# Kernel tuning notes

Hardware: AMD Instinct MI355X
Metric: run time of the kernel (lower is better)

Reference implementation:

```python
import jax, jax.numpy as jnp
import numpy as np

LEAKY_SLOPE = 0.01  # torch F.leaky_relu default
COS_EPS = 1e-8      # torch F.cosine_similarity default eps


def _gc(pre, cur, adj, W):
    # GraphConvolution.forward
    pre_w = pre @ W            # [N, d]
    cur_w = cur @ W            # [M, d]
    new_pre = adj @ cur_w      # [N, d]
    new_cur = adj.T @ pre_w    # [M, d]
    new_pre = jnp.where(new_pre >= 0, new_pre, LEAKY_SLOPE * new_pre)
    new_cur = jnp.where(new_cur >= 0, new_cur, LEAKY_SLOPE * new_cur)
    return new_pre, new_cur


def _cos_sim(pre, cur):
    # Fused pairwise cosine similarity: matches torch F.cosine_similarity per pair
    dots = pre @ cur.T                         # [N, M]
    n_pre = jnp.linalg.norm(pre, axis=1)       # [N]
    n_cur = jnp.linalg.norm(cur, axis=1)       # [M]
    denom = jnp.maximum(n_pre[:, None] * n_cur[None, :], COS_EPS)
    return dots / denom


def setup_inputs() -> dict:
    key = jax.random.key(0)
    k1, k2, k3, k4, k5 = jax.random.split(key, 5)
    N, d = 8192, 128
    stdv = 1.0 / np.sqrt(d)
    pre = jax.random.normal(k1, (N, d), dtype=jnp.float32)
    cur = jax.random.normal(k2, (N, d), dtype=jnp.float32)
    adj = jax.random.uniform(k3, (N, N), dtype=jnp.float32)
    W1 = jax.random.uniform(k4, (d, d), dtype=jnp.float32, minval=-stdv, maxval=stdv)
    W2 = jax.random.uniform(k5, (d, d), dtype=jnp.float32, minval=-stdv, maxval=stdv)
    return {"pre": pre, "cur": cur, "adj": adj, "W1": W1, "W2": W2}


def reference(pre, cur, adj, W1, W2):
    pre1, cur1 = _gc(pre, cur, adj, W1)
    adj1 = _cos_sim(pre1, cur1)
    pre2, cur2 = _gc(pre1, cur1, adj1, W2)
    adj2 = _cos_sim(pre2, cur2)
    return adj2
```

## Files before the change

kernel.cpp:

```cpp
#include <hip/hip_runtime.h>


#define NN 8192
#define DD 128

typedef __bf16 bf16x8 __attribute__((ext_vector_type(8)));
typedef float f32x4 __attribute__((ext_vector_type(4)));

static __device__ __forceinline__ float4 ldg4(const float* p) {
    return *reinterpret_cast<const float4*>(p);
}

static __device__ __forceinline__ unsigned f2bf2(float lo, float hi) {
    __bf16 a = (__bf16)lo, b = (__bf16)hi;
    unsigned short ua = __builtin_bit_cast(unsigned short, a);
    unsigned short ub = __builtin_bit_cast(unsigned short, b);
    return (unsigned)ua | ((unsigned)ub << 16);
}

#define FC(v, j) ((j) == 0 ? (v).x : (j) == 1 ? (v).y : (j) == 2 ? (v).z : (v).w)

#define PRAGU _Pragma("unroll")

static __device__ __forceinline__ int swz16(int row) {
    return (((row & 7) ^ ((row >> 3) & 7)) << 4);
}
static __device__ __forceinline__ int lslot(int row, int slot) {
    return ((slot & 8) << 4) | (((slot & 7) << 4) ^ swz16(row));
}

__global__ __launch_bounds__(256, 2)
void mfma_adj(const float* __restrict__ adj,
              const unsigned short* __restrict__ BTa,
              const unsigned short* __restrict__ BTb,
              float* __restrict__ C, int ksplit, int zstride)
{
    __shared__ alignas(16) char smem[65536];
    char* smA = smem;
    char* smB = smem + 32768;

    const int t    = threadIdx.x;
    const int l    = t & 63;
    const int w    = t >> 6;
    const int wr   = (w >> 1) * 64;
    const int wc   = (w & 1) * 64;
    const int lrow = l & 15;
    const int lhi  = l >> 4;
    const int i0   = blockIdx.x * 128;
    const int z    = blockIdx.z;
    const bool second = z >= 8;
    const unsigned short* BT = second ? BTb : BTa;
    const int kbase = (z & 7) * ksplit;
    C += (size_t)z * (size_t)zstride;

    const int srow = t >> 3;
    const int skg  = t & 7;
    const int u    = t & 31;
    const int r8   = t >> 5;

    f32x4 acc[4][4];
    PRAGU
    for (int r = 0; r < 4; ++r)
        PRAGU
        for (int q = 0; q < 4; ++q)
            PRAGU
            for (int e = 0; e < 4; ++e) acc[r][q][e] = 0.0f;

    const int nt = ksplit >> 7;
    for (int tc = 0; tc < nt; ++tc) {
        const int kk = kbase + tc * 128;

        PRAGU
        for (int h = 0; h < 2; ++h) {
            const int kh = kk + h * 64;
            if (second) {
                float4 rv[8];
                PRAGU
                for (int e = 0; e < 8; ++e)
                    rv[e] = ldg4(&adj[(size_t)(kh + r8 * 8 + e) * NN + i0 + u * 4]);
                PRAGU
                for (int j = 0; j < 4; ++j) {
                    const int c = u * 4 + j;
                    uint4 wv;
                    wv.x = f2bf2(FC(rv[0], j), FC(rv[1], j));
                    wv.y = f2bf2(FC(rv[2], j), FC(rv[3], j));
                    wv.z = f2bf2(FC(rv[4], j), FC(rv[5], j));
                    wv.w = f2bf2(FC(rv[6], j), FC(rv[7], j));
                    *reinterpret_cast<uint4*>(smA + c * 256 + lslot(c, h * 8 + r8)) = wv;
                }
            } else {
                PRAGU
                for (int it = 0; it < 4; ++it) {
                    const int row = it * 32 + srow;
                    const float* g = adj + (size_t)(i0 + row) * NN + kh + skg * 8;
                    float4 f0 = ldg4(g), f1 = ldg4(g + 4);
                    uint4 wv;
                    wv.x = f2bf2(f0.x, f0.y);
                    wv.y = f2bf2(f0.z, f0.w);
                    wv.z = f2bf2(f1.x, f1.y);
                    wv.w = f2bf2(f1.z, f1.w);
                    *reinterpret_cast<uint4*>(smA + row * 256 + lslot(row, h * 8 + skg)) = wv;
                }
            }
            PRAGU
            for (int it = 0; it < 4; ++it) {
                const int n = it * 32 + srow;
                *reinterpret_cast<uint4*>(smB + n * 256 + lslot(n, h * 8 + skg)) =
                    *reinterpret_cast<const uint4*>(BT + (size_t)n * NN + kh + skg * 8);
            }
        }
        __syncthreads();

        PRAGU
        for (int s = 0; s < 4; ++s) {
            bf16x8 af[4], bq[4];
            PRAGU
            for (int r = 0; r < 4; ++r) {
                const int row = wr + r * 16 + lrow;
                af[r] = *reinterpret_cast<const bf16x8*>(smA + row * 256 + lslot(row, s * 4 + lhi));
            }
            PRAGU
            for (int q = 0; q < 4; ++q) {
                const int col = wc + q * 16 + lrow;
                bq[q] = *reinterpret_cast<const bf16x8*>(smB + col * 256 + lslot(col, s * 4 + lhi));
            }
            PRAGU
            for (int r = 0; r < 4; ++r)
                PRAGU
                for (int q = 0; q < 4; ++q)
                    acc[r][q] = __builtin_amdgcn_mfma_f32_16x16x32_bf16(af[r], bq[q], acc[r][q], 0, 0, 0);
        }
        __syncthreads();
    }

    float* sC = (float*)smem;
    PRAGU
    for (int h = 0; h < 2; ++h) {
        if ((w & 1) == h) {
            PRAGU
            for (int r = 0; r < 4; ++r)
                PRAGU
                for (int q = 0; q < 4; ++q)
                    PRAGU
                    for (int i = 0; i < 4; ++i)
                        sC[(wr + r * 16 + lhi * 4 + i) * 68 + q * 16 + lrow] = acc[r][q][i];
        }
        __syncthreads();
        PRAGU
        for (int it = 0; it < 8; ++it) {
            const int idx = it * 256 + t;
            const int row = idx >> 4;
            const int c4  = (idx & 15) << 2;
            f32x4 v = *reinterpret_cast<const f32x4*>(&sC[row * 68 + c4]);
            *reinterpret_cast<f32x4*>(&C[(size_t)(i0 + row) * DD + h * 64 + c4]) = v;
        }
        __syncthreads();
    }
}

__global__ __launch_bounds__(256, 2)
void mfma_out(const unsigned short* __restrict__ A,
              const unsigned short* __restrict__ BT,
              float* __restrict__ C)
{
    __shared__ alignas(16) char smem[65536];
    char* smA = smem;
    char* smB = smem + 32768;

    const int t    = threadIdx.x;
    const int l    = t & 63;
    const int w    = t >> 6;
    const int wr   = (w >> 1) * 64;
    const int wc   = (w & 1) * 64;
    const int lrow = l & 15;
    const int lhi  = l >> 4;
    const int i0   = blockIdx.x * 128;
    const int j0   = blockIdx.y * 128;
    const int s16  = t >> 4;
    const int slot = t & 15;

    f32x4 acc[4][4];
    PRAGU
    for (int r = 0; r < 4; ++r)
        PRAGU
        for (int q = 0; q < 4; ++q)
            PRAGU
            for (int e = 0; e < 4; ++e) acc[r][q][e] = 0.0f;

    PRAGU
    for (int it = 0; it < 8; ++it) {
        const int row = it * 16 + s16;
        *reinterpret_cast<uint4*>(smA + row * 256 + lslot(row, slot)) =
            *reinterpret_cast<const uint4*>(A + (size_t)(i0 + row) * DD + slot * 8);
        *reinterpret_cast<uint4*>(smB + row * 256 + lslot(row, slot)) =
            *reinterpret_cast<const uint4*>(BT + (size_t)(j0 + row) * DD + slot * 8);
    }
    __syncthreads();

    PRAGU
    for (int s = 0; s < 4; ++s) {
        bf16x8 af[4], bq[4];
        PRAGU
        for (int r = 0; r < 4; ++r) {
            const int row = wr + r * 16 + lrow;
            af[r] = *reinterpret_cast<const bf16x8*>(smA + row * 256 + lslot(row, s * 4 + lhi));
        }
        PRAGU
        for (int q = 0; q < 4; ++q) {
            const int col = wc + q * 16 + lrow;
            bq[q] = *reinterpret_cast<const bf16x8*>(smB + col * 256 + lslot(col, s * 4 + lhi));
        }
        PRAGU
        for (int r = 0; r < 4; ++r)
            PRAGU
            for (int q = 0; q < 4; ++q)
                acc[r][q] = __builtin_amdgcn_mfma_f32_16x16x32_bf16(af[r], bq[q], acc[r][q], 0, 0, 0);
    }

    PRAGU
    for (int r = 0; r < 4; ++r)
        PRAGU
        for (int i = 0; i < 4; ++i) {
            const int grow = i0 + wr + r * 16 + lhi * 4 + i;
            float* cp = C + (size_t)grow * NN + j0 + wc;
            PRAGU
            for (int q = 0; q < 4; ++q)
                cp[q * 16 + lrow] = acc[r][q][i];
        }
}

__global__ __launch_bounds__(256, 2)
void gemm_w1t(const float* __restrict__ pre, const float* __restrict__ cur,
              const float* __restrict__ W1,
              unsigned short* __restrict__ pwT, unsigned short* __restrict__ cwT)
{
    __shared__ float sA[32][68];
    __shared__ float sB[64][128];

    const int t  = threadIdx.x;
    const int ct = t & 31;
    const int rt = t >> 5;
    const int bx = blockIdx.x;
    const bool isCur = bx >= 256;
    const float* A = isCur ? cur : pre;
    unsigned short* XT = isCur ? cwT : pwT;
    const int i0 = (bx & 255) * 32;

    float4 acc[4];
    #pragma unroll
    for (int r = 0; r < 4; ++r) { acc[r].x = 0.f; acc[r].y = 0.f; acc[r].z = 0.f; acc[r].w = 0.f; }

    for (int k0 = 0; k0 < DD; k0 += 64) {
        #pragma unroll
        for (int f = 0; f < 2; ++f) {
            const int row = (t >> 4) + 16 * f;
            const int kk4 = (t & 15) << 2;
            *reinterpret_cast<float4*>(&sA[row][kk4]) =
                ldg4(&A[(size_t)(i0 + row) * DD + k0 + kk4]);
        }
        #pragma unroll
        for (int f = 0; f < 8; ++f) {
            const int idx = f * 256 + t;
            const int kk  = idx >> 5;
            const int c4  = (idx & 31) << 2;
            *reinterpret_cast<float4*>(&sB[kk][c4]) =
                ldg4(&W1[(size_t)(k0 + kk) * DD + c4]);
        }
        __syncthreads();
        #pragma unroll 4
        for (int kk = 0; kk < 64; kk += 4) {
            float4 a[4], b[4];
            #pragma unroll
            for (int r = 0; r < 4; ++r)
                a[r] = *reinterpret_cast<const float4*>(&sA[rt * 4 + r][kk]);
            #pragma unroll
            for (int q = 0; q < 4; ++q)
                b[q] = *reinterpret_cast<const float4*>(&sB[kk + q][ct * 4]);
            #pragma unroll
            for (int r = 0; r < 4; ++r) {
                acc[r].x += a[r].x * b[0].x; acc[r].y += a[r].x * b[0].y;
                acc[r].z += a[r].x * b[0].z; acc[r].w += a[r].x * b[0].w;
                acc[r].x += a[r].y * b[1].x; acc[r].y += a[r].y * b[1].y;
                acc[r].z += a[r].y * b[1].z; acc[r].w += a[r].y * b[1].w;
                acc[r].x += a[r].z * b[2].x; acc[r].y += a[r].z * b[2].y;
                acc[r].z += a[r].z * b[2].z; acc[r].w += a[r].z * b[2].w;
                acc[r].x += a[r].w * b[3].x; acc[r].y += a[r].w * b[3].y;
                acc[r].z += a[r].w * b[3].z; acc[r].w += a[r].w * b[3].w;
            }
        }
        __syncthreads();
    }

    float* sC = &sB[0][0];
    #pragma unroll
    for (int r = 0; r < 4; ++r)
        *reinterpret_cast<float4*>(&sC[(rt * 4 + r) * 128 + ct * 4]) = acc[r];
    __syncthreads();

    const int n = t & 127;
    const int g = t >> 7;
    #pragma unroll
    for (int c = 0; c < 2; ++c) {
        const int ii = (2 * g + c) * 8;
        uint4 wv;
        wv.x = f2bf2(sC[(ii + 0) * 128 + n], sC[(ii + 1) * 128 + n]);
        wv.y = f2bf2(sC[(ii + 2) * 128 + n], sC[(ii + 3) * 128 + n]);
        wv.z = f2bf2(sC[(ii + 4) * 128 + n], sC[(ii + 5) * 128 + n]);
        wv.w = f2bf2(sC[(ii + 6) * 128 + n], sC[(ii + 7) * 128 + n]);
        *reinterpret_cast<uint4*>(&XT[(size_t)n * NN + i0 + ii]) = wv;
    }
}

__global__ __launch_bounds__(128)
void rln(const float* __restrict__ kparts, float* __restrict__ Xbase,
         float* __restrict__ invbase)
{
    const int i = blockIdx.x;
    const int y = blockIdx.y;
    const int t = threadIdx.x;
    const float* part = kparts + (size_t)(1 - y) * 8 * (NN * DD);
    float* X = Xbase + (size_t)y * (NN * DD);
    float* inv_n = invbase + y * NN;

    float s = 0.f;
    #pragma unroll
    for (int z = 0; z < 8; ++z)
        s += part[(size_t)z * (NN * DD) + (size_t)i * DD + t];
    float y_ = (s >= 0.f) ? s : 0.01f * s;
    X[(size_t)i * DD + t] = y_;
    float n = y_ * y_;
    #pragma unroll
    for (int o = 32; o > 0; o >>= 1) n += __shfl_down(n, o);
    __shared__ float p[2];
    if ((t & 63) == 0) p[t >> 6] = n;
    __syncthreads();
    if (t == 0) inv_n[i] = 1.0f / sqrtf(p[0] + p[1]);
}

template<bool TRANSA, bool SCALEK, int EPI>
__global__ __launch_bounds__(256, 2)
void gemm32(const float* __restrict__ A, int lda,
            const float* __restrict__ B, int ldb,
            float* __restrict__ C, unsigned short* __restrict__ Cb,
            int ksplit_len, int zstride,
            const float* __restrict__ kscale,
            const float* __restrict__ rscale,
            int ystA, int ystB, int ystC, int ystS)
{
    __shared__ float sA[32][68];
    __shared__ float sB[64][128];

    const int t  = threadIdx.x;
    const int ct = t & 31;
    const int rt = t >> 5;
    const int i0 = blockIdx.x * 32;
    const int side = blockIdx.y;
    const int kgbase = blockIdx.z * ksplit_len;

    A += (ptrdiff_t)side * ystA;
    B += (ptrdiff_t)side * ystB;
    if constexpr (EPI == 0)
        C += (ptrdiff_t)side * ystC + (size_t)blockIdx.z * (size_t)zstride;
    if constexpr (EPI == 3)
        Cb += (ptrdiff_t)side * ystC;
    if constexpr (SCALEK) kscale += (ptrdiff_t)side * ystS;
    if constexpr (EPI == 3) rscale += (ptrdiff_t)side * ystS;

    float4 acc[4];
    #pragma unroll
    for (int r = 0; r < 4; ++r) { acc[r].x = 0.f; acc[r].y = 0.f; acc[r].z = 0.f; acc[r].w = 0.f; }

    for (int k0 = 0; k0 < ksplit_len; k0 += 64) {
        const int kg = kgbase + k0;
        if (!TRANSA) {
            #pragma unroll
            for (int f = 0; f < 2; ++f) {
                const int row = (t >> 4) + 16 * f;
                const int kk4 = (t & 15) << 2;
                *reinterpret_cast<float4*>(&sA[row][kk4]) =
                    ldg4(&A[(size_t)(i0 + row) * lda + kg + kk4]);
            }
        } else {
            #pragma unroll
            for (int f = 0; f < 2; ++f) {
                const int kk = (t >> 3) + 32 * f;
                const int r4 = (t & 7) << 2;
                float4 v = ldg4(&A[(size_t)(kg + kk) * lda + i0 + r4]);
                if (SCALEK) {
                    const float s = kscale[kg + kk];
                    v.x *= s; v.y *= s; v.z *= s; v.w *= s;
                }
                sA[r4 + 0][kk] = v.x; sA[r4 + 1][kk] = v.y;
                sA[r4 + 2][kk] = v.z; sA[r4 + 3][kk] = v.w;
            }
        }
        #pragma unroll
        for (int f = 0; f < 8; ++f) {
            const int idx = f * 256 + t;
            const int kk  = idx >> 5;
            const int c4  = (idx & 31) << 2;
            *reinterpret_cast<float4*>(&sB[kk][c4]) =
                ldg4(&B[(size_t)(kg + kk) * ldb + c4]);
        }
        __syncthreads();
        #pragma unroll 4
        for (int kk = 0; kk < 64; kk += 4) {
            float4 a[4], b[4];
            #pragma unroll
            for (int r = 0; r < 4; ++r)
                a[r] = *reinterpret_cast<const float4*>(&sA[rt * 4 + r][kk]);
            #pragma unroll
            for (int q = 0; q < 4; ++q)
                b[q] = *reinterpret_cast<const float4*>(&sB[kk + q][ct * 4]);
            #pragma unroll
            for (int r = 0; r < 4; ++r) {
                acc[r].x += a[r].x * b[0].x; acc[r].y += a[r].x * b[0].y;
                acc[r].z += a[r].x * b[0].z; acc[r].w += a[r].x * b[0].w;
                acc[r].x += a[r].y * b[1].x; acc[r].y += a[r].y * b[1].y;
                acc[r].z += a[r].y * b[1].z; acc[r].w += a[r].y * b[1].w;
                acc[r].x += a[r].z * b[2].x; acc[r].y += a[r].z * b[2].y;
                acc[r].z += a[r].z * b[2].z; acc[r].w += a[r].z * b[2].w;
                acc[r].x += a[r].w * b[3].x; acc[r].y += a[r].w * b[3].y;
                acc[r].z += a[r].w * b[3].z; acc[r].w += a[r].w * b[3].w;
            }
        }
        __syncthreads();
    }

    #pragma unroll
    for (int r = 0; r < 4; ++r) {
        const int rg = i0 + rt * 4 + r;
        if constexpr (EPI == 3) {
            const float s = rscale[rg];
            float y0 = acc[r].x * s, y1 = acc[r].y * s,
                  y2 = acc[r].z * s, y3 = acc[r].w * s;
            y0 = (y0 >= 0.f) ? y0 : 0.01f * y0;
            y1 = (y1 >= 0.f) ? y1 : 0.01f * y1;
            y2 = (y2 >= 0.f) ? y2 : 0.01f * y2;
            y3 = (y3 >= 0.f) ? y3 : 0.01f * y3;
            float ss = y0 * y0 + y1 * y1 + y2 * y2 + y3 * y3;
            #pragma unroll
            for (int m = 16; m > 0; m >>= 1) ss += __shfl_xor(ss, m);
            const float invn = rsqrtf(ss);
            uint2 wv;
            wv.x = f2bf2(y0 * invn, y1 * invn);
            wv.y = f2bf2(y2 * invn, y3 * invn);
            *reinterpret_cast<uint2*>(&Cb[(size_t)rg * DD + ct * 4]) = wv;
        } else {
            *reinterpret_cast<float4*>(&C[(size_t)rg * DD + ct * 4]) = acc[r];
        }
    }
}

__global__ __launch_bounds__(256)
void reduce_mcmp(const float* __restrict__ part, float* __restrict__ out)
{
    const int y = blockIdx.y;
    const int i = blockIdx.x * 256 + threadIdx.x;
    part += (size_t)y * 32 * 16384;
    out  += (size_t)y * 16384;
    float a = 0.f;
    #pragma unroll
    for (int z = 0; z < 32; ++z) a += part[(size_t)z * 16384 + i];
    out[i] = a;
}

extern "C" void kernel_launch(void* const* d_in, const int* in_sizes, int n_in,
                              void* d_out, int out_size, void* d_ws, size_t ws_size,
                              hipStream_t stream)
{
    const float* pre = (const float*)d_in[0];
    const float* cur = (const float*)d_in[1];
    const float* adj = (const float*)d_in[2];
    const float* W1  = (const float*)d_in[3];
    const float* W2  = (const float*)d_in[4];
    float* out = (float*)d_out;
    float* ws  = (float*)d_ws;

    const size_t M1 = (size_t)NN * DD;

    float* cwpw2 = ws + 0 * M1;
    float* c1    = ws + 2 * M1;
    unsigned short* c2n_b = (unsigned short*)(ws + 4 * M1);
    unsigned short* p2n_b = c2n_b + M1;
    unsigned short* cwT_b = (unsigned short*)(ws + 5 * M1);
    unsigned short* pwT_b = cwT_b + M1;
    float* bparts = ws + 6 * M1;
    float* mcmp   = ws + 7 * M1;
    float* inc1   = mcmp + 32768;
    float* kparts = ws + 8 * M1;

    gemm_w1t<<<dim3(512,1,1),256,0,stream>>>(pre, cur, W1, pwT_b, cwT_b);

    mfma_adj<<<dim3(64,1,16),256,0,stream>>>(adj, cwT_b, pwT_b,
                                             kparts, NN/8, (int)M1);

    rln<<<dim3(NN,2,1),128,0,stream>>>(kparts, c1, inc1);

    gemm32<false,false,0><<<dim3(512,1,1),256,0,stream>>>(
        c1, DD, W2, DD, cwpw2, (unsigned short*)nullptr,
        DD, 0, nullptr, nullptr, 0,0,0,0);

    gemm32<true,true,0><<<dim3(4,2,32),256,0,stream>>>(
        c1, DD, cwpw2, DD, bparts, (unsigned short*)nullptr,
        256, 16384, inc1, nullptr,
        (int)M1, (int)M1, 32*16384, NN);

    reduce_mcmp<<<dim3(64,2,1),256,0,stream>>>(bparts, mcmp);

    gemm32<false,false,3><<<dim3(256,2,1),256,0,stream>>>(
        c1, DD, mcmp + 16384, DD, (float*)nullptr, c2n_b,
        DD, 0, nullptr, inc1,
        (int)M1, -16384, (int)M1, NN);

    mfma_out<<<dim3(64,64,1),256,0,stream>>>(p2n_b, c2n_b, out);
}
```

Measured before the change: 300.3 us.

## Enlarge MFMA block tiles to 256 with 512 threads and 64-wide K steps

Both bf16 MFMA kernels (adjacency GEMM and final cosine output GEMM) now use 512-thread blocks with 256-row tiles; the output kernel also widens to 256 columns with a 4x8 accumulator per wave. The K stage shrinks from 128 to 64 with a simpler 8-slot XOR swizzle, and the adjacency kernel drops its LDS-staged epilogue in favour of direct stores. The goal is better operand reuse per global load and fewer blocks. The cost is higher register pressure, more barriers per K, and less coalesced partial-result stores.

After: 304.8 us. About the same (+1.5%).

```diff
diff --git a/kernel.cpp b/kernel.cpp
--- a/kernel.cpp
+++ b/kernel.cpp
@@ -22,20 +22,17 @@
 
 #define PRAGU _Pragma("unroll")
 
-static __device__ __forceinline__ int swz16(int row) {
-    return (((row & 7) ^ ((row >> 3) & 7)) << 4);
-}
-static __device__ __forceinline__ int lslot(int row, int slot) {
-    return ((slot & 8) << 4) | (((slot & 7) << 4) ^ swz16(row));
-}
-
-__global__ __launch_bounds__(256, 2)
+static __device__ __forceinline__ int lslot8(int row, int slot) {
+    return (((slot ^ (row & 7) ^ ((row >> 3) & 7)) & 7) << 4);
+}
+
+__global__ __launch_bounds__(512, 2)
 void mfma_adj(const float* __restrict__ adj,
               const unsigned short* __restrict__ BTa,
               const unsigned short* __restrict__ BTb,
               float* __restrict__ C, int ksplit, int zstride)
 {
-    __shared__ alignas(16) char smem[65536];
+    __shared__ alignas(16) char smem[49152];
     char* smA = smem;
     char* smB = smem + 32768;
 
@@ -46,17 +43,15 @@
     const int wc   = (w & 1) * 64;
     const int lrow = l & 15;
     const int lhi  = l >> 4;
-    const int i0   = blockIdx.x * 128;
+    const int i0   = blockIdx.x * 256;
     const int z    = blockIdx.z;
     const bool second = z >= 8;
     const unsigned short* BT = second ? BTb : BTa;
     const int kbase = (z & 7) * ksplit;
     C += (size_t)z * (size_t)zstride;
 
-    const int srow = t >> 3;
-    const int skg  = t & 7;
-    const int u    = t & 31;
-    const int r8   = t >> 5;
+    const int u  = t & 63;
+    const int r8 = t >> 6;
 
     f32x4 acc[4][4];
     PRAGU
@@ -66,63 +61,62 @@
             PRAGU
             for (int e = 0; e < 4; ++e) acc[r][q][e] = 0.0f;
 
-    const int nt = ksplit >> 7;
-    for (int tc = 0; tc < nt; ++tc) {
-        const int kk = kbase + tc * 128;
-
-        PRAGU
-        for (int h = 0; h < 2; ++h) {
-            const int kh = kk + h * 64;
-            if (second) {
-                float4 rv[8];
-                PRAGU
-                for (int e = 0; e < 8; ++e)
-                    rv[e] = ldg4(&adj[(size_t)(kh + r8 * 8 + e) * NN + i0 + u * 4]);
-                PRAGU
-                for (int j = 0; j < 4; ++j) {
-                    const int c = u * 4 + j;
-                    uint4 wv;
-                    wv.x = f2bf2(FC(rv[0], j), FC(rv[1], j));
-                    wv.y = f2bf2(FC(rv[2], j), FC(rv[3], j));
-                    wv.z = f2bf2(FC(rv[4], j), FC(rv[5], j));
-                    wv.w = f2bf2(FC(rv[6], j), FC(rv[7], j));
-                    *reinterpret_cast<uint4*>(smA + c * 256 + lslot(c, h * 8 + r8)) = wv;
-                }
-            } else {
-                PRAGU
-                for (int it = 0; it < 4; ++it) {
-                    const int row = it * 32 + srow;
-                    const float* g = adj + (size_t)(i0 + row) * NN + kh + skg * 8;
-                    float4 f0 = ldg4(g), f1 = ldg4(g + 4);
-                    uint4 wv;
-                    wv.x = f2bf2(f0.x, f0.y);
-                    wv.y = f2bf2(f0.z, f0.w);
-                    wv.z = f2bf2(f1.x, f1.y);
-                    wv.w = f2bf2(f1.z, f1.w);
-                    *reinterpret_cast<uint4*>(smA + row * 256 + lslot(row, h * 8 + skg)) = wv;
-                }
-            }
+    for (int k0 = 0; k0 < ksplit; k0 += 64) {
+        const int kk = kbase + k0;
+
+        if (second) {
+            float4 rv[8];
+            PRAGU
+            for (int e = 0; e < 8; ++e)
+                rv[e] = ldg4(&adj[(size_t)(kk + r8 * 8 + e) * NN + i0 + u * 4]);
+            PRAGU
+            for (int j = 0; j < 4; ++j) {
+                const int c = u * 4 + j;
+                uint4 wv;
+                wv.x = f2bf2(FC(rv[0], j), FC(rv[1], j));
+                wv.y = f2bf2(FC(rv[2], j), FC(rv[3], j));
+                wv.z = f2bf2(FC(rv[4], j), FC(rv[5], j));
+                wv.w = f2bf2(FC(rv[6], j), FC(rv[7], j));
+                *reinterpret_cast<uint4*>(smA + c * 128 + lslot8(c, r8)) = wv;
+            }
+        } else {
             PRAGU
             for (int it = 0; it < 4; ++it) {
-                const int n = it * 32 + srow;
-                *reinterpret_cast<uint4*>(smB + n * 256 + lslot(n, h * 8 + skg)) =
-                    *reinterpret_cast<const uint4*>(BT + (size_t)n * NN + kh + skg * 8);
-            }
-        }
-        __syncthreads();
-
-        PRAGU
-        for (int s = 0; s < 4; ++s) {
+                const int row  = it * 64 + (t >> 3);
+                const int slot = t & 7;
+                const float* g = adj + (size_t)(i0 + row) * NN + kk + slot * 8;
+                float4 f0 = ldg4(g), f1 = ldg4(g + 4);
+                uint4 wv;
+                wv.x = f2bf2(f0.x, f0.y);
+                wv.y = f2bf2(f0.z, f0.w);
+                wv.z = f2bf2(f1.x, f1.y);
+                wv.w = f2bf2(f1.z, f1.w);
+                *reinterpret_cast<uint4*>(smA + row * 128 + lslot8(row, slot)) = wv;
+            }
+        }
+
+        PRAGU
+        for (int it = 0; it < 2; ++it) {
+            const int idx  = it * 512 + t;
+            const int n    = idx >> 3;
+            const int slot = idx & 7;
+            *reinterpret_cast<uint4*>(smB + n * 128 + lslot8(n, slot)) =
+                *reinterpret_cast<const uint4*>(BT + (size_t)n * NN + kk + slot * 8);
+        }
+        __syncthreads();
+
+        PRAGU
+        for (int s = 0; s < 2; ++s) {
             bf16x8 af[4], bq[4];
             PRAGU
             for (int r = 0; r < 4; ++r) {
                 const int row = wr + r * 16 + lrow;
-                af[r] = *reinterpret_cast<const bf16x8*>(smA + row * 256 + lslot(row, s * 4 + lhi));
+                af[r] = *reinterpret_cast<const bf16x8*>(smA + row * 128 + lslot8(row, s * 4 + lhi));
             }
             PRAGU
             for (int q = 0; q < 4; ++q) {
                 const int col = wc + q * 16 + lrow;
-                bq[q] = *reinterpret_cast<const bf16x8*>(smB + col * 256 + lslot(col, s * 4 + lhi));
+                bq[q] = *reinterpret_cast<const bf16x8*>(smB + col * 128 + lslot8(col, s * 4 + lhi));
             }
             PRAGU
             for (int r = 0; r < 4; ++r)
@@ -133,32 +127,19 @@
         __syncthreads();
     }
 
-    float* sC = (float*)smem;
     PRAGU
-    for (int h = 0; h < 2; ++h) {
-        if ((w & 1) == h) {
-            PRAGU
-            for (int r = 0; r < 4; ++r)
-                PRAGU
-                for (int q = 0; q < 4; ++q)
-                    PRAGU
-                    for (int i = 0; i < 4; ++i)
-                        sC[(wr + r * 16 + lhi * 4 + i) * 68 + q * 16 + lrow] = acc[r][q][i];
-        }
-        __syncthreads();
-        PRAGU
-        for (int it = 0; it < 8; ++it) {
-            const int idx = it * 256 + t;
-            const int row = idx >> 4;
-            const int c4  = (idx & 15) << 2;
-            f32x4 v = *reinterpret_cast<const f32x4*>(&sC[row * 68 + c4]);
-            *reinterpret_cast<f32x4*>(&C[(size_t)(i0 + row) * DD + h * 64 + c4]) = v;
-        }
-        __syncthreads();
-    }
-}
-
-__global__ __launch_bounds__(256, 2)
+    for (int r = 0; r < 4; ++r)
+        PRAGU
+        for (int i = 0; i < 4; ++i) {
+            const int grow = i0 + wr + r * 16 + lhi * 4 + i;
+            float* cp = C + (size_t)grow * DD + wc;
+            PRAGU
+            for (int q = 0; q < 4; ++q)
+                cp[q * 16 + lrow] = acc[r][q][i];
+        }
+}
+
+__global__ __launch_bounds__(512, 2)
 void mfma_out(const unsigned short* __restrict__ A,
               const unsigned short* __restrict__ BT,
               float* __restrict__ C)
@@ -171,50 +152,53 @@
     const int l    = t & 63;
     const int w    = t >> 6;
     const int wr   = (w >> 1) * 64;
-    const int wc   = (w & 1) * 64;
+    const int wc   = (w & 1) * 128;
     const int lrow = l & 15;
     const int lhi  = l >> 4;
-    const int i0   = blockIdx.x * 128;
-    const int j0   = blockIdx.y * 128;
-    const int s16  = t >> 4;
-    const int slot = t & 15;
-
-    f32x4 acc[4][4];
+    const int i0   = blockIdx.x * 256;
+    const int j0   = blockIdx.y * 256;
+
+    f32x4 acc[4][8];
     PRAGU
     for (int r = 0; r < 4; ++r)
         PRAGU
-        for (int q = 0; q < 4; ++q)
+        for (int q = 0; q < 8; ++q)
             PRAGU
             for (int e = 0; e < 4; ++e) acc[r][q][e] = 0.0f;
 
     PRAGU
-    for (int it = 0; it < 8; ++it) {
-        const int row = it * 16 + s16;
-        *reinterpret_cast<uint4*>(smA + row * 256 + lslot(row, slot)) =
-            *reinterpret_cast<const uint4*>(A + (size_t)(i0 + row) * DD + slot * 8);
-        *reinterpret_cast<uint4*>(smB + row * 256 + lslot(row, slot)) =
-            *reinterpret_cast<const uint4*>(BT + (size_t)(j0 + row) * DD + slot * 8);
-    }
-    __syncthreads();
-
-    PRAGU
-    for (int s = 0; s < 4; ++s) {
-        bf16x8 af[4], bq[4];
-        PRAGU
-        for (int r = 0; r < 4; ++r) {
-            const int row = wr + r * 16 + lrow;
-            af[r] = *reinterpret_cast<const bf16x8*>(smA + row * 256 + lslot(row, s * 4 + lhi));
-        }
-        PRAGU
-        for (int q = 0; q < 4; ++q) {
-            const int col = wc + q * 16 + lrow;
-            bq[q] = *reinterpret_cast<const bf16x8*>(smB + col * 256 + lslot(col, s * 4 + lhi));
-        }
-        PRAGU
-        for (int r = 0; r < 4; ++r)
-            PRAGU
-            for (int q = 0; q < 4; ++q)
-                acc[r][q] = __builtin_amdgcn_mfma_f32_16x16x32_bf16(af[r], bq[q], acc[r][q], 0, 0, 0);
+    for (int ks = 0; ks < 2; ++ks) {
+        if (ks) __syncthreads();
+        PRAGU
+        for (int it = 0; it < 4; ++it) {
+            const int row  = it * 64 + (t >> 3);
+            const int slot = t & 7;
+            *reinterpret_cast<uint4*>(smA + row * 128 + lslot8(row, slot)) =
+                *reinterpret_cast<const uint4*>(A + (size_t)(i0 + row) * DD + ks * 64 + slot * 8);
+            *reinterpret_cast<uint4*>(smB + row * 128 + lslot8(row, slot)) =
+                *reinterpret_cast<const uint4*>(BT + (size_t)(j0 + row) * DD + ks * 64 + slot * 8);
+        }
+        __syncthreads();
+
+        PRAGU
+        for (int s = 0; s < 2; ++s) {
+            bf16x8 af[4], bq[8];
+            PRAGU
+            for (int r = 0; r < 4; ++r) {
+                const int row = wr + r * 16 + lrow;
+                af[r] = *reinterpret_cast<const bf16x8*>(smA + row * 128 + lslot8(row, s * 4 + lhi));
+            }
+            PRAGU
+            for (int q = 0; q < 8; ++q) {
+                const int col = wc + q * 16 + lrow;
+                bq[q] = *reinterpret_cast<const bf16x8*>(smB + col * 128 + lslot8(col, s * 4 + lhi));
+            }
+            PRAGU
+            for (int r = 0; r < 4; ++r)
+                PRAGU
+                for (int q = 0; q < 8; ++q)
+                    acc[r][q] = __builtin_amdgcn_mfma_f32_16x16x32_bf16(af[r], bq[q], acc[r][q], 0, 0, 0);
+        }
     }
 
     PRAGU
@@ -224,7 +208,7 @@
             const int grow = i0 + wr + r * 16 + lhi * 4 + i;
             float* cp = C + (size_t)grow * NN + j0 + wc;
             PRAGU
-            for (int q = 0; q < 4; ++q)
+            for (int q = 0; q < 8; ++q)
                 cp[q * 16 + lrow] = acc[r][q][i];
         }
 }
@@ -492,7 +476,7 @@
 
     gemm_w1t<<<dim3(512,1,1),256,0,stream>>>(pre, cur, W1, pwT_b, cwT_b);
 
-    mfma_adj<<<dim3(64,1,16),256,0,stream>>>(adj, cwT_b, pwT_b,
+    mfma_adj<<<dim3(32,1,16),512,0,stream>>>(adj, cwT_b, pwT_b,
                                              kparts, NN/8, (int)M1);
 
     rln<<<dim3(NN,2,1),128,0,stream>>>(kparts, c1, inc1);
@@ -513,5 +497,5 @@
         DD, 0, nullptr, inc1,
         (int)M1, -16384, (int)M1, NN);
 
-    mfma_out<<<dim3(64,64,1),256,0,stream>>>(p2n_b, c2n_b, out);
-}
+    mfma_out<<<dim3(32,32,1),512,0,stream>>>(p2n_b, c2n_b, out);
+}
```

## Load GEMM tiles straight to LDS with global_load_lds and convert fp32 on read

Applied to the files above, without the earlier changes.

The adj GEMM and output GEMM now use the buffer-to-LDS direct load (global_load_lds, 16 bytes) with XOR-swizzled layouts, instead of loading into registers and storing to shared memory. The fp32 adj tile is kept in fp32 in LDS and converted to bf16 when fragments are read, with the K tile cut to 64. This frees registers and LDS so launch bounds rise to 3 blocks per CU. The epilogue now writes the accumulators directly rather than staging them through LDS. The risks are more LDS reads per MFMA because of the fp32 staging, uncoalesced output stores, and no double buffering to overlap the direct loads.

New measurement: 380.5 us. +26.7%, slower.

```diff
diff --git a/kernel.cpp b/kernel.cpp
--- a/kernel.cpp
+++ b/kernel.cpp
@@ -6,6 +6,9 @@
 
 typedef __bf16 bf16x8 __attribute__((ext_vector_type(8)));
 typedef float f32x4 __attribute__((ext_vector_type(4)));
+
+typedef __attribute__((address_space(3))) void lds_void;
+typedef const __attribute__((address_space(1))) void gbl_void;
 
 static __device__ __forceinline__ float4 ldg4(const float* p) {
     return *reinterpret_cast<const float4*>(p);
@@ -18,24 +21,21 @@
     return (unsigned)ua | ((unsigned)ub << 16);
 }
 
-#define FC(v, j) ((j) == 0 ? (v).x : (j) == 1 ? (v).y : (j) == 2 ? (v).z : (v).w)
-
 #define PRAGU _Pragma("unroll")
 
-static __device__ __forceinline__ int swz16(int row) {
-    return (((row & 7) ^ ((row >> 3) & 7)) << 4);
-}
-static __device__ __forceinline__ int lslot(int row, int slot) {
-    return ((slot & 8) << 4) | (((slot & 7) << 4) ^ swz16(row));
-}
-
-__global__ __launch_bounds__(256, 2)
+static __device__ __forceinline__ void gl16(const void* g, char* lbase, int loff) {
+    loff = __builtin_amdgcn_readfirstlane(loff);
+    __builtin_amdgcn_global_load_lds((gbl_void*)g, (lds_void*)(lbase + loff),
+                                     16, 0, 0);
+}
+
+__global__ __launch_bounds__(256, 3)
 void mfma_adj(const float* __restrict__ adj,
               const unsigned short* __restrict__ BTa,
               const unsigned short* __restrict__ BTb,
               float* __restrict__ C, int ksplit, int zstride)
 {
-    __shared__ alignas(16) char smem[65536];
+    __shared__ alignas(16) char smem[49152];
     char* smA = smem;
     char* smB = smem + 32768;
 
@@ -53,11 +53,6 @@
     const int kbase = (z & 7) * ksplit;
     C += (size_t)z * (size_t)zstride;
 
-    const int srow = t >> 3;
-    const int skg  = t & 7;
-    const int u    = t & 31;
-    const int r8   = t >> 5;
-
     f32x4 acc[4][4];
     PRAGU
     for (int r = 0; r < 4; ++r)
@@ -66,63 +61,79 @@
             PRAGU
             for (int e = 0; e < 4; ++e) acc[r][q][e] = 0.0f;
 
-    const int nt = ksplit >> 7;
-    for (int tc = 0; tc < nt; ++tc) {
-        const int kk = kbase + tc * 128;
-
-        PRAGU
-        for (int h = 0; h < 2; ++h) {
-            const int kh = kk + h * 64;
+    const int nt = ksplit >> 6;
+    for (int tt = 0; tt < nt; ++tt) {
+        const int kk = kbase + tt * 64;
+
+        if (second) {
+            PRAGU
+            for (int it = 0; it < 8; ++it) {
+                const int krow  = (w * 8 + it) * 2 + (l >> 5);
+                const int g = (l & 31) ^ ((krow & 7) ^ ((krow >> 3) & 7));
+                gl16(adj + (size_t)(kk + krow) * NN + i0 + g * 4,
+                     smA, (w * 8 + it) * 1024);
+            }
+        } else {
+            PRAGU
+            for (int it = 0; it < 8; ++it) {
+                const int row = (w * 8 + it) * 4 + (l >> 4);
+                const int g   = (l & 15) ^ (row & 15);
+                gl16(adj + (size_t)(i0 + row) * NN + kk + g * 4,
+                     smA, (w * 8 + it) * 1024);
+            }
+        }
+        PRAGU
+        for (int it = 0; it < 4; ++it) {
+            const int n = (w * 4 + it) * 8 + (l >> 3);
+            const int g = (l & 7) ^ (n & 7);
+            gl16(BT + (size_t)n * NN + kk + g * 8,
+                 smB, (w * 4 + it) * 1024);
+        }
+        __syncthreads();
+
+        PRAGU
+        for (int s = 0; s < 2; ++s) {
+            bf16x8 af[4], bq[4];
             if (second) {
-                float4 rv[8];
                 PRAGU
-                for (int e = 0; e < 8; ++e)
-                    rv[e] = ldg4(&adj[(size_t)(kh + r8 * 8 + e) * NN + i0 + u * 4]);
-                PRAGU
-                for (int j = 0; j < 4; ++j) {
-                    const int c = u * 4 + j;
-                    uint4 wv;
-                    wv.x = f2bf2(FC(rv[0], j), FC(rv[1], j));
-                    wv.y = f2bf2(FC(rv[2], j), FC(rv[3], j));
-                    wv.z = f2bf2(FC(rv[4], j), FC(rv[5], j));
-                    wv.w = f2bf2(FC(rv[6], j), FC(rv[7], j));
-                    *reinterpret_cast<uint4*>(smA + c * 256 + lslot(c, h * 8 + r8)) = wv;
+                for (int r = 0; r < 4; ++r) {
+                    const int i  = wr + r * 16 + lrow;
+                    const int ic = i >> 2;
+                    const int ib = (i & 3) * 4;
+                    float v[8];
+                    PRAGU
+                    for (int j = 0; j < 8; ++j) {
+                        const int k = s * 32 + lhi * 8 + j;
+                        const int p = (k & 7) ^ ((k >> 3) & 7);
+                        v[j] = *reinterpret_cast<const float*>(
+                            smA + k * 512 + ((ic ^ p) << 4) + ib);
+                    }
+                    union { unsigned u[4]; bf16x8 h; } cv;
+                    cv.u[0] = f2bf2(v[0], v[1]); cv.u[1] = f2bf2(v[2], v[3]);
+                    cv.u[2] = f2bf2(v[4], v[5]); cv.u[3] = f2bf2(v[6], v[7]);
+                    af[r] = cv.h;
                 }
             } else {
                 PRAGU
-                for (int it = 0; it < 4; ++it) {
-                    const int row = it * 32 + srow;
-                    const float* g = adj + (size_t)(i0 + row) * NN + kh + skg * 8;
-                    float4 f0 = ldg4(g), f1 = ldg4(g + 4);
-                    uint4 wv;
-                    wv.x = f2bf2(f0.x, f0.y);
-                    wv.y = f2bf2(f0.z, f0.w);
-                    wv.z = f2bf2(f1.x, f1.y);
-                    wv.w = f2bf2(f1.z, f1.w);
-                    *reinterpret_cast<uint4*>(smA + row * 256 + lslot(row, h * 8 + skg)) = wv;
+                for (int r = 0; r < 4; ++r) {
+                    const int row = wr + r * 16 + lrow;
+                    const int c   = s * 8 + lhi * 2;
+                    f32x4 a0 = *reinterpret_cast<const f32x4*>(
+                        smA + row * 256 + (((c    ) ^ (row & 15)) << 4));
+                    f32x4 a1 = *reinterpret_cast<const f32x4*>(
+                        smA + row * 256 + (((c + 1) ^ (row & 15)) << 4));
+                    union { unsigned u[4]; bf16x8 h; } cv;
+                    cv.u[0] = f2bf2(a0[0], a0[1]); cv.u[1] = f2bf2(a0[2], a0[3]);
+                    cv.u[2] = f2bf2(a1[0], a1[1]); cv.u[3] = f2bf2(a1[2], a1[3]);
+                    af[r] = cv.h;
                 }
             }
             PRAGU
-            for (int it = 0; it < 4; ++it) {
-                const int n = it * 32 + srow;
-                *reinterpret_cast<uint4*>(smB + n * 256 + lslot(n, h * 8 + skg)) =
-                    *reinterpret_cast<const uint4*>(BT + (size_t)n * NN + kh + skg * 8);
-            }
-        }
-        __syncthreads();
-
-        PRAGU
-        for (int s = 0; s < 4; ++s) {
-            bf16x8 af[4], bq[4];
-            PRAGU
-            for (int r = 0; r < 4; ++r) {
-                const int row = wr + r * 16 + lrow;
-                af[r] = *reinterpret_cast<const bf16x8*>(smA + row * 256 + lslot(row, s * 4 + lhi));
-            }
-            PRAGU
             for (int q = 0; q < 4; ++q) {
-                const int col = wc + q * 16 + lrow;
-                bq[q] = *reinterpret_cast<const bf16x8*>(smB + col * 256 + lslot(col, s * 4 + lhi));
+                const int n = wc + q * 16 + lrow;
+                const int c = s * 4 + lhi;
+                bq[q] = *reinterpret_cast<const bf16x8*>(
+                    smB + n * 128 + ((c ^ (n & 7)) << 4));
             }
             PRAGU
             for (int r = 0; r < 4; ++r)
@@ -133,29 +144,16 @@
         __syncthreads();
     }
 
-    float* sC = (float*)smem;
     PRAGU
-    for (int h = 0; h < 2; ++h) {
-        if ((w & 1) == h) {
-            PRAGU
-            for (int r = 0; r < 4; ++r)
-                PRAGU
-                for (int q = 0; q < 4; ++q)
-                    PRAGU
-                    for (int i = 0; i < 4; ++i)
-                        sC[(wr + r * 16 + lhi * 4 + i) * 68 + q * 16 + lrow] = acc[r][q][i];
-        }
-        __syncthreads();
-        PRAGU
-        for (int it = 0; it < 8; ++it) {
-            const int idx = it * 256 + t;
-            const int row = idx >> 4;
-            const int c4  = (idx & 15) << 2;
-            f32x4 v = *reinterpret_cast<const f32x4*>(&sC[row * 68 + c4]);
-            *reinterpret_cast<f32x4*>(&C[(size_t)(i0 + row) * DD + h * 64 + c4]) = v;
-        }
-        __syncthreads();
-    }
+    for (int r = 0; r < 4; ++r)
+        PRAGU
+        for (int i = 0; i < 4; ++i) {
+            const int grow = i0 + wr + r * 16 + lhi * 4 + i;
+            float* cp = C + (size_t)grow * DD + wc;
+            PRAGU
+            for (int q = 0; q < 4; ++q)
+                cp[q * 16 + lrow] = acc[r][q][i];
+        }
 }
 
 __global__ __launch_bounds__(256, 2)
@@ -176,8 +174,6 @@
     const int lhi  = l >> 4;
     const int i0   = blockIdx.x * 128;
     const int j0   = blockIdx.y * 128;
-    const int s16  = t >> 4;
-    const int slot = t & 15;
 
     f32x4 acc[4][4];
     PRAGU
@@ -189,11 +185,10 @@
 
     PRAGU
     for (int it = 0; it < 8; ++it) {
-        const int row = it * 16 + s16;
-        *reinterpret_cast<uint4*>(smA + row * 256 + lslot(row, slot)) =
-            *reinterpret_cast<const uint4*>(A + (size_t)(i0 + row) * DD + slot * 8);
-        *reinterpret_cast<uint4*>(smB + row * 256 + lslot(row, slot)) =
-            *reinterpret_cast<const uint4*>(BT + (size_t)(j0 + row) * DD + slot * 8);
+        const int row = (w * 8 + it) * 4 + (l >> 4);
+        const int g   = (l & 15) ^ (row & 15);
+        gl16(A  + (size_t)(i0 + row) * DD + g * 8, smA, (w * 8 + it) * 1024);
+        gl16(BT + (size_t)(j0 + row) * DD + g * 8, smB, (w * 8 + it) * 1024);
     }
     __syncthreads();
 
@@ -203,12 +198,16 @@
         PRAGU
         for (int r = 0; r < 4; ++r) {
             const int row = wr + r * 16 + lrow;
-            af[r] = *reinterpret_cast<const bf16x8*>(smA + row * 256 + lslot(row, s * 4 + lhi));
+            const int c   = s * 4 + lhi;
+            af[r] = *reinterpret_cast<const bf16x8*>(
+                smA + row * 256 + ((c ^ (row & 15)) << 4));
         }
         PRAGU
         for (int q = 0; q < 4; ++q) {
-            const int col = wc + q * 16 + lrow;
-            bq[q] = *reinterpret_cast<const bf16x8*>(smB + col * 256 + lslot(col, s * 4 + lhi));
+            const int n = wc + q * 16 + lrow;
+            const int c = s * 4 + lhi;
+            bq[q] = *reinterpret_cast<const bf16x8*>(
+                smB + n * 256 + ((c ^ (n & 15)) << 4));
         }
         PRAGU
         for (int r = 0; r < 4; ++r)
```
